# Kernel optimization log

Measured on AMD Instinct MI355X. Metric: run time of the kernel, lower is better.

Reference implementation:

```python
import jax, jax.numpy as jnp
import numpy as np

GRAY_THRESHOLD = 127.5  # undefined global in source; midpoint of [0,255] implied by Convert_to_0_255
N_BINS = 512            # 3x3 binary pattern -> codes 0..511
DILATION = 1

# LBP-style fixed conv weights: powers of two laid out row-major
_LBP_W = jnp.array([[256., 128., 64.],
                    [32.,  16.,  8.],
                    [4.,   2.,   1.]], dtype=jnp.float32).reshape(1, 1, 3, 3)  # OIHW


def _pattern_hist(img):
    # img: [N,1,H,W] in [-1,1]-ish range
    x = (img * 0.5 + 0.5) * 255.0          # Convert_to_0_255
    b = (x > GRAY_THRESHOLD).astype(jnp.float32)  # binarize
    # 3x3 valid conv with dilation encodes each 3x3 binary neighborhood as an int code 0..511
    codes = jax.lax.conv_general_dilated(
        b, _LBP_W, window_strides=(1, 1), padding='VALID',
        rhs_dilation=(DILATION, DILATION),
        dimension_numbers=('NCHW', 'OIHW', 'NCHW'))
    idx = codes.reshape(-1).astype(jnp.int32)  # exact integers, int cast == torch .int()
    n = idx.shape[0]
    counts = jnp.zeros((N_BINS,), jnp.float32).at[idx].add(1.0)  # bincount(minlength=512)
    return counts / n


def setup_inputs() -> dict:
    key = jax.random.key(0)
    k1, k2 = jax.random.split(key)
    input = jax.random.normal(k1, (64, 1, 512, 512), dtype=jnp.float32)
    target = jax.random.normal(k2, (64, 1, 512, 512), dtype=jnp.float32)
    return {"input": input, "target": target}


def reference(input, target):
    N, C, H, W = input.shape
    h_in = _pattern_hist(input)
    h_tgt = _pattern_hist(target)
    s = jnp.mean((h_in - h_tgt) ** 2)  # nn.MSELoss
    return s / N / C
```

## Files before the change

kernel.cpp:

```cpp
#include <hip/hip_runtime.h>
#include <stdint.h>

#define HH 512
#define WW 512
#define NIMG 64
#define OH 510
#define OW 510
#define NB 512
#define SEGR 16
#define NSEG 32
#define NREP 64
#define BLOCK 256
#define NBIG (NIMG * 2 * NSEG * 2)
#define NSEAM (NIMG * 2 * 8)
#define NBLK ((NBIG + NSEAM) / 4)
#define HBINS 576

typedef float f4 __attribute__((ext_vector_type(4)));

__device__ __forceinline__ f4 ldg4(const float* addr) {
    f4 r;
    asm volatile("global_load_dwordx4 %0, %1, off" : "=v"(r) : "v"(addr));
    return r;
}
template<int N>
__device__ __forceinline__ void waitv(f4& x) {
    if      constexpr (N == 7) asm volatile("s_waitcnt vmcnt(7)" : "+v"(x));
    else if constexpr (N == 6) asm volatile("s_waitcnt vmcnt(6)" : "+v"(x));
    else if constexpr (N == 5) asm volatile("s_waitcnt vmcnt(5)" : "+v"(x));
    else if constexpr (N == 4) asm volatile("s_waitcnt vmcnt(4)" : "+v"(x));
    else if constexpr (N == 3) asm volatile("s_waitcnt vmcnt(3)" : "+v"(x));
    else if constexpr (N == 2) asm volatile("s_waitcnt vmcnt(2)" : "+v"(x));
    else if constexpr (N == 1) asm volatile("s_waitcnt vmcnt(1)" : "+v"(x));
    else                       asm volatile("s_waitcnt vmcnt(0)" : "+v"(x));
}

#define BINC 0x1p-24f

__device__ __forceinline__ int pack4(f4 v) {
    return (v.x > BINC) | ((v.y > BINC) << 1) | ((v.z > BINC) << 2) | ((v.w > BINC) << 3);
}

__global__ __launch_bounds__(BLOCK) void hist_kernel(const float* __restrict__ inp,
                                                     const float* __restrict__ tgt,
                                                     int* __restrict__ rep) {
    __shared__ int hist[HBINS];
    const int tid  = threadIdx.x;
    const int lane = tid & 63;
    const int wave = tid >> 6;

    for (int i = tid; i < HBINS; i += BLOCK) hist[i] = 0;
    __syncthreads();

    const int task  = blockIdx.x * 4 + wave;
    const int dummy = 512 + lane;

    if (task < NBIG) {
        const int tile = task & 1;
        const int seg  = (task >> 1) & 31;
        const int t    = (task >> 6) & 1;
        const int img  = task >> 7;
        const int r0   = seg * SEGR;
        const int R    = min(SEGR, OH - r0);
        const int c0   = tile * 256 + 4 * lane;
        const int sign = 1 - 2 * t;
        const float* base = (t ? tgt : inp) + (size_t)img * (HH * WW) + c0;
        auto ap = [&](int rel) { return base + (size_t)min(r0 + rel, HH - 1) * WW; };

        f4 X[8];
        #pragma unroll
        for (int k = 0; k < 8; ++k) X[k] = ldg4(ap(k));

        int n0, n1, n2;
        waitv<7>(X[0]);
        { int nib = pack4(X[0]); n0 = nib | (__shfl_down(nib, 1) << 4); }
        X[0] = ldg4(ap(8));
        waitv<7>(X[1]);
        { int nib = pack4(X[1]); n1 = nib | (__shfl_down(nib, 1) << 4); }
        X[1] = ldg4(ap(9));

        #define STEP(o, W) { \
            f4& Xs = X[((o) + 2) & 7]; \
            waitv<W>(Xs); \
            int nib = pack4(Xs); \
            n2 = nib | (__shfl_down(nib, 1) << 4); \
            if ((o) <= 7) Xs = ldg4(ap((o) + 10)); \
            if ((o) < R) { \
                _Pragma("unroll") \
                for (int j = 0; j < 4; ++j) { \
                    int code = ((n0 >> j) & 7) | (((n1 >> j) & 7) << 3) \
                             | (((n2 >> j) & 7) << 6); \
                    int slot = (lane < 63 || j < 2) ? code : dummy; \
                    atomicAdd(&hist[slot], sign); \
                } \
            } \
            n0 = n1; n1 = n2; }

        STEP(0, 7)  STEP(1, 7)  STEP(2, 7)  STEP(3, 7)
        STEP(4, 7)  STEP(5, 7)  STEP(6, 7)  STEP(7, 7)
        STEP(8, 7)  STEP(9, 6)  STEP(10, 5) STEP(11, 4)
        STEP(12, 3) STEP(13, 2) STEP(14, 1) STEP(15, 0)
        #undef STEP
    } else {
        const int idx = task - NBIG;
        const int seg = idx & 7;
        const int t   = (idx >> 3) & 1;
        const int img = idx >> 4;
        const int sign = 1 - 2 * t;
        const int r   = seg * 64 + lane;
        const bool v  = (r < OH);
        const float* bp = (t ? tgt : inp) + (size_t)img * (HH * WW);
        int p[3];
        #pragma unroll
        for (int k = 0; k < 3; ++k) {
            const float* rowp = bp + (size_t)min(r + k, HH - 1) * WW;
            float2 A = *(const float2*)(rowp + 254);
            float2 B = *(const float2*)(rowp + 256);
            p[k] = (A.x > BINC) | ((A.y > BINC) << 1)
                 | ((B.x > BINC) << 2) | ((B.y > BINC) << 3);
        }
        int c254 = (p[0] & 7) | ((p[1] & 7) << 3) | ((p[2] & 7) << 6);
        int c255 = ((p[0] >> 1) & 7) | (((p[1] >> 1) & 7) << 3) | (((p[2] >> 1) & 7) << 6);
        atomicAdd(&hist[v ? c254 : dummy], sign);
        atomicAdd(&hist[v ? c255 : dummy], sign);
    }

    __syncthreads();
    const int rid = blockIdx.x & (NREP - 1);
    for (int i = tid; i < NB; i += BLOCK) {
        int vv = hist[i];
        if (vv) atomicAdd(&rep[rid * NB + i], vv);
    }
}

__global__ __launch_bounds__(NB) void reduce_kernel(const int* __restrict__ rep,
                                                    float* __restrict__ out) {
    __shared__ double sdata[NB];
    int tid = threadIdx.x;
    int s = 0;
    #pragma unroll
    for (int r = 0; r < NREP; ++r) s += rep[r * NB + tid];
    double d = (double)s;
    sdata[tid] = d * d;
    __syncthreads();
    for (int stp = NB / 2; stp > 0; stp >>= 1) {
        if (tid < stp) sdata[tid] += sdata[tid + stp];
        __syncthreads();
    }
    if (tid == 0) {
        const double n = (double)NIMG * OH * OW;
        out[0] = (float)(sdata[0] / (n * n) / 512.0 / 64.0);
    }
}

extern "C" void kernel_launch(void* const* d_in, const int* in_sizes, int n_in,
                              void* d_out, int out_size, void* d_ws, size_t ws_size,
                              hipStream_t stream) {
    const float* inp = (const float*)d_in[0];
    const float* tgt = (const float*)d_in[1];
    float* out = (float*)d_out;
    int* rep = (int*)d_ws;

    hipMemsetAsync(rep, 0, NREP * NB * sizeof(int), stream);
    hist_kernel<<<NBLK, BLOCK, 0, stream>>>(inp, tgt, rep);
    reduce_kernel<<<1, NB, 0, stream>>>(rep, out);
}
```

Baseline: 151.3 us.

## Histogram 3x4 pair patterns into 4096 bins and expand in reduce

Each atomic now records a 12-bit 3x4 window code that covers two adjacent 3x3 LBP codes, which halves the LDS atomics. The reduce kernel splits each pair bin back into its two 9-bit codes. Blocks are enlarged to 512 threads with a fixed grid of 512 blocks, each wave looping over two tasks, and the seam tasks are folded into every fourth wave. The trade is a larger LDS histogram, a longer 4096-bin flush to global memory, and fewer replicas (8), so global atomic contention in the flush is higher.

```diff
diff --git a/kernel.cpp b/kernel.cpp
--- a/kernel.cpp
+++ b/kernel.cpp
@@ -6,15 +6,17 @@
 #define NIMG 64
 #define OH 510
 #define OW 510
-#define NB 512
+#define NPB 4096
+#define HBINS (NPB + 64)
 #define SEGR 16
 #define NSEG 32
-#define NREP 64
-#define BLOCK 256
+#define NREP 8
+#define BLOCK 512
+#define WPB (BLOCK / 64)
+#define NBLK 512
+#define NWAVE (NBLK * WPB)
 #define NBIG (NIMG * 2 * NSEG * 2)
 #define NSEAM (NIMG * 2 * 8)
-#define NBLK ((NBIG + NSEAM) / 4)
-#define HBINS 576
 
 typedef float f4 __attribute__((ext_vector_type(4)));
 
@@ -52,10 +54,13 @@
     for (int i = tid; i < HBINS; i += BLOCK) hist[i] = 0;
     __syncthreads();
 
-    const int task  = blockIdx.x * 4 + wave;
-    const int dummy = 512 + lane;
+    const int wid   = blockIdx.x * WPB + wave;
+    const int dummy = NPB + ((lane + wave * 8) & 63);
+    const bool ln_ok = (lane < 63);
 
-    if (task < NBIG) {
+    #pragma unroll 1
+    for (int k = 0; k < 2; ++k) {
+        const int task = wid + k * NWAVE;
         const int tile = task & 1;
         const int seg  = (task >> 1) & 31;
         const int t    = (task >> 6) & 1;
@@ -69,7 +74,7 @@
 
         f4 X[8];
         #pragma unroll
-        for (int k = 0; k < 8; ++k) X[k] = ldg4(ap(k));
+        for (int q = 0; q < 8; ++q) X[q] = ldg4(ap(q));
 
         int n0, n1, n2;
         waitv<7>(X[0]);
@@ -86,13 +91,11 @@
             n2 = nib | (__shfl_down(nib, 1) << 4); \
             if ((o) <= 7) Xs = ldg4(ap((o) + 10)); \
             if ((o) < R) { \
-                _Pragma("unroll") \
-                for (int j = 0; j < 4; ++j) { \
-                    int code = ((n0 >> j) & 7) | (((n1 >> j) & 7) << 3) \
-                             | (((n2 >> j) & 7) << 6); \
-                    int slot = (lane < 63 || j < 2) ? code : dummy; \
-                    atomicAdd(&hist[slot], sign); \
-                } \
+                int p01 = (n0 & 15) | ((n1 & 15) << 4) | ((n2 & 15) << 8); \
+                int p23 = ((n0 >> 2) & 15) | (((n1 >> 2) & 15) << 4) \
+                        | (((n2 >> 2) & 15) << 8); \
+                atomicAdd(&hist[p01], sign); \
+                atomicAdd(&hist[ln_ok ? p23 : dummy], sign); \
             } \
             n0 = n1; n1 = n2; }
 
@@ -101,8 +104,10 @@
         STEP(8, 7)  STEP(9, 6)  STEP(10, 5) STEP(11, 4)
         STEP(12, 3) STEP(13, 2) STEP(14, 1) STEP(15, 0)
         #undef STEP
-    } else {
-        const int idx = task - NBIG;
+    }
+
+    if ((wid & 3) == 0) {
+        const int idx = wid >> 2;
         const int seg = idx & 7;
         const int t   = (idx >> 3) & 1;
         const int img = idx >> 4;
@@ -112,44 +117,57 @@
         const float* bp = (t ? tgt : inp) + (size_t)img * (HH * WW);
         int p[3];
         #pragma unroll
-        for (int k = 0; k < 3; ++k) {
-            const float* rowp = bp + (size_t)min(r + k, HH - 1) * WW;
+        for (int q = 0; q < 3; ++q) {
+            const float* rowp = bp + (size_t)min(r + q, HH - 1) * WW;
             float2 A = *(const float2*)(rowp + 254);
             float2 B = *(const float2*)(rowp + 256);
-            p[k] = (A.x > BINC) | ((A.y > BINC) << 1)
+            p[q] = (A.x > BINC) | ((A.y > BINC) << 1)
                  | ((B.x > BINC) << 2) | ((B.y > BINC) << 3);
         }
-        int c254 = (p[0] & 7) | ((p[1] & 7) << 3) | ((p[2] & 7) << 6);
-        int c255 = ((p[0] >> 1) & 7) | (((p[1] >> 1) & 7) << 3) | (((p[2] >> 1) & 7) << 6);
-        atomicAdd(&hist[v ? c254 : dummy], sign);
-        atomicAdd(&hist[v ? c255 : dummy], sign);
+        int pair = p[0] | (p[1] << 4) | (p[2] << 8);
+        atomicAdd(&hist[v ? pair : dummy], sign);
     }
 
     __syncthreads();
     const int rid = blockIdx.x & (NREP - 1);
-    for (int i = tid; i < NB; i += BLOCK) {
+    for (int i = tid; i < NPB; i += BLOCK) {
         int vv = hist[i];
-        if (vv) atomicAdd(&rep[rid * NB + i], vv);
+        if (vv) atomicAdd(&rep[rid * NPB + i], vv);
     }
 }
 
-__global__ __launch_bounds__(NB) void reduce_kernel(const int* __restrict__ rep,
-                                                    float* __restrict__ out) {
-    __shared__ double sdata[NB];
-    int tid = threadIdx.x;
-    int s = 0;
+__global__ __launch_bounds__(1024) void reduce_kernel(const int* __restrict__ rep,
+                                                      float* __restrict__ out) {
+    __shared__ int sh[512];
+    __shared__ double sd[512];
+    const int tid = threadIdx.x;
+    if (tid < 512) sh[tid] = 0;
+    __syncthreads();
+
     #pragma unroll
-    for (int r = 0; r < NREP; ++r) s += rep[r * NB + tid];
-    double d = (double)s;
-    sdata[tid] = d * d;
+    for (int k = 0; k < NPB / 1024; ++k) {
+        int p = tid + k * 1024;
+        int s = 0;
+        #pragma unroll
+        for (int r = 0; r < NREP; ++r) s += rep[r * NPB + p];
+        if (s) {
+            int f0 = (p & 7) | (((p >> 4) & 7) << 3) | (((p >> 8) & 7) << 6);
+            int f1 = ((p >> 1) & 7) | (((p >> 5) & 7) << 3) | (((p >> 9) & 7) << 6);
+            atomicAdd(&sh[f0], s);
+            atomicAdd(&sh[f1], s);
+        }
+    }
     __syncthreads();
-    for (int stp = NB / 2; stp > 0; stp >>= 1) {
-        if (tid < stp) sdata[tid] += sdata[tid + stp];
+
+    if (tid < 512) { double d = (double)sh[tid]; sd[tid] = d * d; }
+    __syncthreads();
+    for (int stp = 256; stp > 0; stp >>= 1) {
+        if (tid < stp) sd[tid] += sd[tid + stp];
         __syncthreads();
     }
     if (tid == 0) {
         const double n = (double)NIMG * OH * OW;
-        out[0] = (float)(sdata[0] / (n * n) / 512.0 / 64.0);
+        out[0] = (float)(sd[0] / (n * n) / 512.0 / 64.0);
     }
 }
 
@@ -161,7 +179,7 @@
     float* out = (float*)d_out;
     int* rep = (int*)d_ws;
 
-    hipMemsetAsync(rep, 0, NREP * NB * sizeof(int), stream);
+    hipMemsetAsync(rep, 0, NREP * NPB * sizeof(int), stream);
     hist_kernel<<<NBLK, BLOCK, 0, stream>>>(inp, tgt, rep);
-    reduce_kernel<<<1, NB, 0, stream>>>(rep, out);
+    reduce_kernel<<<1, 1024, 0, stream>>>(rep, out);
 }
```

New measurement: 149.1 us. Within noise of the previous version (-1.5%).
